# Kernel optimization log

Measured on AMD Instinct MI355X. Metric: run time of the kernel, lower is better.

The kernel has to match this reference:

```python
import jax, jax.numpy as jnp
import numpy as np

K = 20          # neighbors
M = 8           # weight-bank size per layer
EPS = 1e-5      # BatchNorm eps


def _bn(x, axes):
    # training-mode BatchNorm at init (gamma=1, beta=0), biased variance like torch
    mu = x.mean(axes, keepdims=True)
    var = x.var(axes, keepdims=True)
    return (x - mu) * jax.lax.rsqrt(var + EPS)


def _gather(feat, idx):
    # feat [B,N,C], idx [B,N,K] -> neighbor features [B,N,K,C]
    return jax.vmap(lambda f, i: f[i])(feat, idx)


def _knn_idx(x):
    # x [B,C,N]; pairwise_distance = -||xi||^2 + 2 xi.xj - ||xj||^2 (neg sq dist)
    sq = jnp.sum(x * x, axis=1)                      # [B,N]
    inner = jnp.einsum('bcn,bcm->bnm', x, x)          # [B,N,N]
    pd = 2.0 * inner - sq[:, :, None] - sq[:, None, :]
    return jax.lax.top_k(pd, K)[1]                    # [B,N,K]


def _scorenet(xyz, w1, w2, b):
    # xyz [B,N,K,6]; 1x1 Conv2d == channel-last matmul; BN2d over (B,N,K)
    h = jax.nn.relu(_bn(xyz @ w1, (0, 1, 2)))         # [B,N,K,16]
    s = h @ w2 + b                                    # [B,N,K,M]
    return jax.nn.softmax(s, axis=-1) + 0.5           # softmax over m, bias=0.5


def _paconv(feat, idx, ker, score):
    # feat [B,N,C]; ker [2C, M*O]; score [B,N,K,M]
    # torch: point = concat(x,x) @ ker -> [B,N,M,O]; center = x @ ker[:C]
    # assemble_dgcnn (assign_score_withk, aggregate='sum'):
    #   out[b,n,o] = sum_{k,m} score[b,n,k,m] * (point[b, idx[b,n,k], m, o] - center[b, n, m, o])
    C = feat.shape[-1]
    k3 = ker.reshape(2 * C, M, -1)
    Wa, Wb = k3[:C], k3[C:]                           # point uses Wa+Wb (x repeated); center uses Wa
    nf = _gather(feat, idx)                           # [B,N,K,C]
    T = jnp.einsum('bnkm,bnkc->bnmc', score, nf)      # score-weighted neighbor feats
    out = jnp.einsum('bnmc,cmo->bno', T, Wa + Wb)
    out = out - jnp.einsum('bnm,bnc,cmo->bno', score.sum(2), feat, Wa)
    return jax.nn.relu(_bn(out, (0, 1)))              # BN1d over (B,N), channel-last


def setup_inputs() -> dict:
    key = jax.random.key(0)
    ks = jax.random.split(key, 18)
    B, N = 32, 1024
    dims = [(3, 64), (64, 64), (64, 128), (128, 256)]
    d = {"x": jax.random.normal(ks[0], (B, 3, N), dtype=jnp.float32)}
    for i, (ci, co) in enumerate(dims):
        scale = (2.0 / (2 * ci)) ** 0.5  # kaiming_normal over fan_in=2*ci
        d[f"mat{i+1}"] = jax.random.normal(ks[1 + i], (2 * ci, M * co), dtype=jnp.float32) * scale
        d[f"sn{i+1}_w1"] = jax.random.normal(ks[5 + i], (6, 16), dtype=jnp.float32) * 0.4
        d[f"sn{i+1}_w2"] = jax.random.normal(ks[9 + i], (16, M), dtype=jnp.float32) * 0.25
        d[f"sn{i+1}_b"] = jnp.zeros((M,), dtype=jnp.float32)
    d["conv5_w"] = jax.random.normal(ks[13], (512, 1024), dtype=jnp.float32) * 0.04
    d["lin1_w"] = jax.random.normal(ks[14], (2048, 512), dtype=jnp.float32) * 0.02
    d["lin2_w"] = jax.random.normal(ks[15], (512, 256), dtype=jnp.float32) * 0.04
    d["lin3_w"] = jax.random.normal(ks[16], (256, 40), dtype=jnp.float32) * 0.06
    d["lin3_b"] = jnp.zeros((40,), dtype=jnp.float32)
    return d


def reference(x, mat1, mat2, mat3, mat4,
              sn1_w1, sn1_w2, sn1_b, sn2_w1, sn2_w2, sn2_b,
              sn3_w1, sn3_w2, sn3_b, sn4_w1, sn4_w2, sn4_b,
              conv5_w, lin1_w, lin2_w, lin3_w, lin3_b):
    idx = _knn_idx(x)                                  # [B,N,K]
    xT = jnp.swapaxes(x, 1, 2)                         # [B,N,3]
    nx = _gather(xT, idx)                              # [B,N,K,3]
    xyz = jnp.concatenate([nx - xT[:, :, None, :], nx], axis=-1)  # [B,N,K,6]

    p1 = _paconv(xT, idx, mat1, _scorenet(xyz, sn1_w1, sn1_w2, sn1_b))  # [B,N,64]
    p2 = _paconv(p1, idx, mat2, _scorenet(xyz, sn2_w1, sn2_w2, sn2_b))  # [B,N,64]
    p3 = _paconv(p2, idx, mat3, _scorenet(xyz, sn3_w1, sn3_w2, sn3_b))  # [B,N,128]
    p4 = _paconv(p3, idx, mat4, _scorenet(xyz, sn4_w1, sn4_w2, sn4_b))  # [B,N,256]

    p = jnp.concatenate([p1, p2, p3, p4], axis=-1)     # [B,N,512]
    p = jax.nn.relu(_bn(p @ conv5_w, (0, 1)))          # [B,N,1024]
    g = jnp.concatenate([p.max(axis=1), p.mean(axis=1)], axis=-1)  # [B,2048]
    h = jax.nn.relu(_bn(g @ lin1_w, (0,)))             # [B,512] (dropout = identity)
    h = jax.nn.relu(_bn(h @ lin2_w, (0,)))             # [B,256]
    return h @ lin3_w + lin3_b                         # [B,40]
```

## Files before the change

kernel.cpp:

```cpp
#include <hip/hip_runtime.h>
#include <cstdint>
#include <cstddef>

static constexpr int Bc  = 32;
static constexpr int Nc  = 1024;
static constexpr int Kc  = 20;
static constexpr int Mc  = 8;
static constexpr int BNc = Bc * Nc;
static constexpr int BNKc = BNc * Kc;

typedef __attribute__((ext_vector_type(4))) float f32x4;
typedef _Float16 f16x8 __attribute__((ext_vector_type(8)));

__device__ inline short f2h(float v) { _Float16 h = (_Float16)v; return __builtin_bit_cast(short, h); }
__device__ inline float h2f(short s) { return (float)__builtin_bit_cast(_Float16, s); }

__global__ void zero_kernel(float* p, int n) {
  int gid = blockIdx.x * blockDim.x + threadIdx.x;
  if (gid < n) p[gid] = 0.f;
}

__global__ __launch_bounds__(256) void knn_kernel(const float* __restrict__ x,
                                                  int* __restrict__ idxout) {
  int wv = threadIdx.x >> 6;
  int bn = blockIdx.x * 4 + wv;
  int b = bn >> 10, n = bn & (Nc - 1);
  int lane = threadIdx.x & 63;
  const float* xb = x + (size_t)b * 3 * Nc;
  float cx = xb[n], cy = xb[Nc + n], cz = xb[2 * Nc + n];
  float sqc = cx * cx + cy * cy + cz * cz;
  float d[16];
#pragma unroll
  for (int j = 0; j < 16; j++) {
    int m2 = j * 64 + lane;
    float xm = xb[m2], ym = xb[Nc + m2], zm = xb[2 * Nc + m2];
    d[j] = 2.f * (cx * xm + cy * ym + cz * zm) - sqc - (xm * xm + ym * ym + zm * zm);
  }
  int* out = idxout + (size_t)bn * Kc;
  for (int kk = 0; kk < Kc; kk++) {
    float bd = d[0]; int bj = 0;
#pragma unroll
    for (int j = 1; j < 16; j++)
      if (d[j] > bd) { bd = d[j]; bj = j; }
    int bm = bj * 64 + lane;
#pragma unroll
    for (int off = 32; off; off >>= 1) {
      float od = __shfl_down(bd, off);
      int   om = __shfl_down(bm, off);
      if (od > bd || (od == bd && om < bm)) { bd = od; bm = om; }
    }
    bm = __shfl(bm, 0);
    if (lane == 0) out[kk] = bm;
    int bmj = bm >> 6;
    bool mine = (bm & 63) == lane;
#pragma unroll
    for (int j = 0; j < 16; j++)
      if (mine && j == bmj) d[j] = -3e38f;
  }
}

__global__ __launch_bounds__(256) void xt_kernel(const float* __restrict__ x,
                                                 float* __restrict__ xT) {
  int gid = blockIdx.x * blockDim.x + threadIdx.x;
  int c = gid % 3;
  int bn = gid / 3;
  int b = bn >> 10, n = bn & (Nc - 1);
  xT[gid] = x[((size_t)b * 3 + c) * Nc + n];
}

__device__ inline void xyz_at(const float* __restrict__ xT, const int* __restrict__ idx,
                              int e, float v[6]) {
  int bn = e / Kc;
  int b = bn >> 10;
  int nb = idx[e];
  const float* pc = xT + (size_t)bn * 3;
  const float* pn = xT + ((size_t)(b << 10) + nb) * 3;
#pragma unroll
  for (int c = 0; c < 3; c++) { float nv = pn[c]; v[c] = nv - pc[c]; v[3 + c] = nv; }
}

__global__ __launch_bounds__(256) void xyz_stats_kernel(const float* __restrict__ xT,
                                                        const int* __restrict__ idx,
                                                        float* __restrict__ accum) {
  __shared__ float sPart[4 * 42];
  int tid = threadIdx.x;
  int gid = blockIdx.x * 256 + tid;
  float a[42];
#pragma unroll
  for (int t = 0; t < 42; t++) a[t] = 0.f;
  for (int i = 0; i < 8; i++) {
    float v[6];
    xyz_at(xT, idx, gid + i * 81920, v);
#pragma unroll
    for (int c = 0; c < 6; c++) a[c] += v[c];
    int t = 6;
#pragma unroll
    for (int c = 0; c < 6; c++)
#pragma unroll
      for (int d = 0; d < 6; d++) a[t++] += v[c] * v[d];
  }
  int lane = tid & 63, wid = tid >> 6;
#pragma unroll
  for (int t = 0; t < 42; t++) {
    float v = a[t];
#pragma unroll
    for (int off = 32; off; off >>= 1) v += __shfl_down(v, off);
    if (lane == 0) sPart[wid * 42 + t] = v;
  }
  __syncthreads();
  if (tid < 42) {
    float s = sPart[tid] + sPart[42 + tid] + sPart[84 + tid] + sPart[126 + tid];
    atomicAdd(&accum[tid], s);
  }
}

__global__ void snstats_kernel(const float* __restrict__ accum,
                               const float* __restrict__ w1a, const float* __restrict__ w1b,
                               const float* __restrict__ w1c, const float* __restrict__ w1d,
                               float* __restrict__ snstats) {
  int t = threadIdx.x;
  int l = t >> 4, j = t & 15;
  const float* w1 = (l == 0) ? w1a : (l == 1) ? w1b : (l == 2) ? w1c : w1d;
  const float invc = 1.f / (float)BNKc;
  float wj[6];
  float mu = 0.f;
#pragma unroll
  for (int c = 0; c < 6; c++) { wj[c] = w1[c * 16 + j]; mu += accum[c] * invc * wj[c]; }
  float e2 = 0.f;
#pragma unroll
  for (int c = 0; c < 6; c++)
#pragma unroll
    for (int d = 0; d < 6; d++) e2 += wj[c] * wj[d] * (accum[6 + c * 6 + d] * invc);
  float var = e2 - mu * mu;
  snstats[t * 2] = mu;
  snstats[t * 2 + 1] = rsqrtf(var + 1e-5f);
}

__global__ __launch_bounds__(256) void score_kernel(const float* __restrict__ xT,
                                                    const int* __restrict__ idx,
                                                    const float* __restrict__ w1,
                                                    const float* __restrict__ w2,
                                                    const float* __restrict__ bias,
                                                    const float* __restrict__ snst,
                                                    float* __restrict__ score) {
  __shared__ float sW1[96], sW2[128], sB[8], sMu[16], sRs[16];
  int tid = threadIdx.x;
  if (tid < 96) sW1[tid] = w1[tid];
  else if (tid < 224) sW2[tid - 96] = w2[tid - 96];
  else if (tid < 232) sB[tid - 224] = bias[tid - 224];
  else if (tid < 248) { sMu[tid - 232] = snst[(tid - 232) * 2]; sRs[tid - 232] = snst[(tid - 232) * 2 + 1]; }
  __syncthreads();
  int e = blockIdx.x * 256 + tid;
  float v[6];
  xyz_at(xT, idx, e, v);
  float h[16];
#pragma unroll
  for (int j = 0; j < 16; j++) {
    float a = 0.f;
#pragma unroll
    for (int c = 0; c < 6; c++) a += v[c] * sW1[c * 16 + j];
    a = (a - sMu[j]) * sRs[j];
    h[j] = a > 0.f ? a : 0.f;
  }
  float s[8];
  float mx = -3e38f;
#pragma unroll
  for (int m = 0; m < 8; m++) {
    float a = sB[m];
#pragma unroll
    for (int j = 0; j < 16; j++) a += h[j] * sW2[j * 8 + m];
    s[m] = a;
    mx = fmaxf(mx, a);
  }
  float sum = 0.f;
#pragma unroll
  for (int m = 0; m < 8; m++) { s[m] = expf(s[m] - mx); sum += s[m]; }
  float inv = 1.f / sum;
#pragma unroll
  for (int m = 0; m < 8; m++) score[(size_t)e * 8 + m] = s[m] * inv + 0.5f;
}

template <int C, int Co, int MH>
__global__ __launch_bounds__(256) void paconv_kernel(
    const float* __restrict__ feat, int fstride,
    const float* __restrict__ ker,
    const float* __restrict__ score,
    const int* __restrict__ idx,
    float* __restrict__ outp, int ostride) {
  constexpr int PT = 8;
  constexpr int MS = Mc / MH;
  __shared__ float sX[PT][2 * MH * C];
  __shared__ float sSc[PT * Kc * Mc];
  __shared__ int sIdx[PT * Kc];
  __shared__ float sFc[PT][C];
  __shared__ float sSum[PT][Mc];

  int tid = threadIdx.x;
  int pbase = blockIdx.x * PT;
  int bN = pbase & ~(Nc - 1);

  for (int e = tid; e < PT * Kc; e += 256) sIdx[e] = idx[(size_t)pbase * Kc + e];
  for (int e = tid; e < PT * Kc * Mc; e += 256) sSc[e] = score[(size_t)pbase * Kc * Mc + e];
  for (int e = tid; e < PT * C; e += 256) {
    int p = e / C, c = e - p * C;
    sFc[p][c] = feat[(size_t)(pbase + p) * fstride + c];
  }
  __syncthreads();
  for (int e = tid; e < PT * Mc; e += 256) {
    int p = e >> 3, m = e & 7;
    float s = 0.f;
#pragma unroll
    for (int k = 0; k < Kc; k++) s += sSc[p * Kc * Mc + k * Mc + m];
    sSum[p][m] = s;
  }
  __syncthreads();

  constexpr int OG = Co;
  constexpr int PG = 256 / OG;
  constexpr int PPT = PT / PG;
  int o = tid % OG;
  int pg = tid / OG;
  float acc[PPT];
#pragma unroll
  for (int i = 0; i < PPT; i++) acc[i] = 0.f;

  for (int ms = 0; ms < MS; ms++) {
    int mb = ms * MH;
    for (int e = tid; e < PT * C; e += 256) {
      int p = e / C, c = e - p * C;
      float t[MH];
#pragma unroll
      for (int mm = 0; mm < MH; mm++) t[mm] = 0.f;
      const float* sc = &sSc[p * Kc * Mc + mb];
      for (int k = 0; k < Kc; k++) {
        float v = feat[(size_t)(bN + sIdx[p * Kc + k]) * fstride + c];
#pragma unroll
        for (int mm = 0; mm < MH; mm++) t[mm] += sc[k * Mc + mm] * v;
      }
      float fc = sFc[p][c];
#pragma unroll
      for (int mm = 0; mm < MH; mm++) {
        sX[p][mm * C + c] = t[mm] - sSum[p][mb + mm] * fc;
        sX[p][MH * C + mm * C + c] = t[mm];
      }
    }
    __syncthreads();
#pragma unroll
    for (int mm = 0; mm < MH; mm++) {
      int m = mb + mm;
      const float* kerm = ker + (size_t)m * Co + o;
      for (int c = 0; c < C; c++) {
        float wA = kerm[(size_t)c * (Mc * Co)];
        float wB = kerm[(size_t)(C + c) * (Mc * Co)];
        int r = mm * C + c;
#pragma unroll
        for (int i = 0; i < PPT; i++) {
          int p = pg * PPT + i;
          acc[i] += sX[p][r] * wA;
          acc[i] += sX[p][MH * C + r] * wB;
        }
      }
    }
    __syncthreads();
  }

#pragma unroll
  for (int i = 0; i < PPT; i++) {
    int p = pg * PPT + i;
    outp[(size_t)(pbase + p) * ostride + o] = acc[i];
  }
}

template <int C>
__global__ __launch_bounds__(256) void gather_kernel(
    const short* __restrict__ pb, int coff,
    const float* __restrict__ score,
    const int* __restrict__ idx,
    short* __restrict__ TU, int p0) {
  constexpr int PT = 256 / C;
  __shared__ float sSc[PT][Kc][Mc];
  __shared__ int   sIdx[PT][Kc];
  __shared__ float sSum[PT][Mc];
  int tid = threadIdx.x;
  int pbase = p0 + blockIdx.x * PT;
  int bbase = pbase & ~(Nc - 1);
  for (int e = tid; e < PT * Kc * Mc; e += 256) (&sSc[0][0][0])[e] = score[(size_t)pbase * Kc * Mc + e];
  for (int e = tid; e < PT * Kc; e += 256) (&sIdx[0][0])[e] = idx[(size_t)pbase * Kc + e];
  __syncthreads();
  if (tid < PT * Mc) {
    int p = tid >> 3, m = tid & 7;
    float s = 0.f;
#pragma unroll
    for (int k = 0; k < Kc; k++) s += sSc[p][k][m];
    sSum[p][m] = s;
  }
  __syncthreads();
  int p = tid / C, c = tid - p * C;
  float t[Mc];
#pragma unroll
  for (int m = 0; m < Mc; m++) t[m] = 0.f;
  for (int k = 0; k < Kc; k++) {
    float v = h2f(pb[(size_t)(bbase + sIdx[p][k]) * 512 + coff + c]);
#pragma unroll
    for (int m = 0; m < Mc; m++) t[m] += sSc[p][k][m] * v;
  }
  float fc = h2f(pb[(size_t)(pbase + p) * 512 + coff + c]);
  short* rowp = TU + (size_t)(pbase + p - p0) * (2 * Mc * C);
#pragma unroll
  for (int m = 0; m < Mc; m++) {
    rowp[m * C + c]          = f2h(t[m] - sSum[p][m] * fc);
    rowp[Mc * C + m * C + c] = f2h(t[m]);
  }
}

__global__ __launch_bounds__(256) void kerconv_kernel(const float* __restrict__ ker,
                                                      short* __restrict__ Bt,
                                                      int C, int Co, int total) {
  int gid = blockIdx.x * 256 + threadIdx.x;
  if (gid >= total) return;
  int RT = 2 * Mc * C;
  int o = gid / RT, r = gid - o * RT;
  int half = r / (Mc * C);
  int mc = r - half * Mc * C;
  int m = mc / C, c = mc - m * C;
  Bt[gid] = f2h(ker[(size_t)(half * C + c) * (Mc * Co) + m * Co + o]);
}

__global__ __launch_bounds__(256) void w5conv_kernel(const float* __restrict__ W,
                                                     short* __restrict__ Wt) {
  int gid = blockIdx.x * 256 + threadIdx.x;
  int o = gid >> 9, k = gid & 511;
  Wt[gid] = f2h(W[(size_t)k * 1024 + o]);
}

template <int BM, int BN, bool OUT_HALF>
__global__ __launch_bounds__(256) void gemm_kernel(
    const short* __restrict__ A,
    const short* __restrict__ Bt,
    int K,
    void* __restrict__ Cout, int ldc) {
  constexpr int BK = 64;
  constexpr int FM = (BM + 31) / 32;
  constexpr int FN = BN / 32;
  __shared__ short sA[BM * BK];
  __shared__ short sB[BN * BK];
  int tid = threadIdx.x;
  int lane = tid & 63, wv = tid >> 6;
  int wrow = (wv & 1) * (BM / 2);
  int wcol = (wv >> 1) * (BN / 2);
  int bm0 = blockIdx.x * BM;
  int bn0 = blockIdx.y * BN;
  int r15 = lane & 15, quad = lane >> 4;
  int swz = r15 & 7;

  constexpr int FMW = BM / 32 >= 1 ? BM / 32 : 1;
  f32x4 acc[FMW][FN];
#pragma unroll
  for (int fm = 0; fm < FMW; fm++)
#pragma unroll
    for (int fn = 0; fn < FN; fn++) acc[fm][fn] = (f32x4){0.f, 0.f, 0.f, 0.f};

  for (int k0 = 0; k0 < K; k0 += BK) {
#pragma unroll
    for (int i = 0; i < (BM * BK / 8) / 256; i++) {
      int cb = i * 256 + wv * 64;
      int chunk = cb + lane;
      int row = chunk >> 3, kc = (chunk & 7) ^ (row & 7);
      const short* g = A + (size_t)(bm0 + row) * K + k0 + kc * 8;
      __builtin_amdgcn_global_load_lds((const __attribute__((address_space(1))) void*)g,
                                       (__attribute__((address_space(3))) void*)&sA[cb * 8],
                                       16, 0, 0);
    }
#pragma unroll
    for (int i = 0; i < (BN * BK / 8) / 256; i++) {
      int cb = i * 256 + wv * 64;
      int chunk = cb + lane;
      int row = chunk >> 3, kc = (chunk & 7) ^ (row & 7);
      const short* g = Bt + (size_t)(bn0 + row) * K + k0 + kc * 8;
      __builtin_amdgcn_global_load_lds((const __attribute__((address_space(1))) void*)g,
                                       (__attribute__((address_space(3))) void*)&sB[cb * 8],
                                       16, 0, 0);
    }
    __syncthreads();
#pragma unroll
    for (int kk = 0; kk < BK; kk += 32) {
      f16x8 af[FMW], bf[FN];
      int ccol = (kk >> 3) + quad;
#pragma unroll
      for (int fm = 0; fm < FMW; fm++)
        af[fm] = *(const f16x8*)&sA[(wrow + fm * 16 + r15) * BK + ((ccol ^ swz) * 8)];
#pragma unroll
      for (int fn = 0; fn < FN; fn++)
        bf[fn] = *(const f16x8*)&sB[(wcol + fn * 16 + r15) * BK + ((ccol ^ swz) * 8)];
#pragma unroll
      for (int fm = 0; fm < FMW; fm++)
#pragma unroll
        for (int fn = 0; fn < FN; fn++)
          acc[fm][fn] = __builtin_amdgcn_mfma_f32_16x16x32_f16(af[fm], bf[fn], acc[fm][fn], 0, 0, 0);
    }
    __syncthreads();
  }

#pragma unroll
  for (int fn = 0; fn < FN; fn++) {
    int col = bn0 + wcol + fn * 16 + r15;
#pragma unroll
    for (int fm = 0; fm < FMW; fm++) {
      int rowb = bm0 + wrow + fm * 16 + quad * 4;
#pragma unroll
      for (int r = 0; r < 4; r++) {
        float v = acc[fm][fn][r];
        if constexpr (OUT_HALF) ((short*)Cout)[(size_t)(rowb + r) * ldc + col] = f2h(v);
        else                    ((float*)Cout)[(size_t)(rowb + r) * ldc + col] = v;
      }
    }
  }
}

template <bool IS_HALF>
__global__ __launch_bounds__(256) void bnstats_kernel(const void* __restrict__ pre,
                                                      int Co,
                                                      float* __restrict__ bnslots) {
  __shared__ float sS[4][64], sQ[4][64];
  int tid = threadIdx.x;
  int c = tid & 63, tg = tid >> 6;
  int ch = blockIdx.x * 64 + c;
  int row0 = blockIdx.y * 1024 + tg * 256;
  float s = 0.f, q = 0.f;
  if constexpr (IS_HALF) {
    const short* p = (const short*)pre + (size_t)row0 * Co + ch;
#pragma unroll 4
    for (int r = 0; r < 256; r++) {
      float v = h2f(p[(size_t)r * Co]);
      s += v; q += v * v;
    }
  } else {
    const float* p = (const float*)pre + (size_t)row0 * Co + ch;
#pragma unroll 4
    for (int r = 0; r < 256; r++) {
      float v = p[(size_t)r * Co];
      s += v; q += v * v;
    }
  }
  sS[tg][c] = s; sQ[tg][c] = q;
  __syncthreads();
  if (tid < 64) {
    float ts = sS[0][tid] + sS[1][tid] + sS[2][tid] + sS[3][tid];
    float tq = sQ[0][tid] + sQ[1][tid] + sQ[2][tid] + sQ[3][tid];
    int chh = blockIdx.x * 64 + tid;
    bnslots[(chh * 32 + blockIdx.y) * 2 + 0] = ts;
    bnslots[(chh * 32 + blockIdx.y) * 2 + 1] = tq;
  }
}

__global__ void bnfinalize_kernel(const float* __restrict__ slots,
                                  float* __restrict__ bnmr, int Co) {
  int ch = blockIdx.x * blockDim.x + threadIdx.x;
  if (ch >= Co) return;
  float s = 0.f, q = 0.f;
#pragma unroll 4
  for (int i = 0; i < 32; i++) { s += slots[(ch * 32 + i) * 2]; q += slots[(ch * 32 + i) * 2 + 1]; }
  float mu = s / (float)BNc;
  float var = q / (float)BNc - mu * mu;
  bnmr[ch * 2] = mu;
  bnmr[ch * 2 + 1] = rsqrtf(var + 1e-5f);
}

__global__ __launch_bounds__(256) void bnapply_kernel(const float* __restrict__ pre,
                                                      int Co, const float* __restrict__ bnmr,
                                                      short* __restrict__ pb, int coff) {
  int gid = blockIdx.x * 256 + threadIdx.x;
  int row = gid / Co, ch = gid - row * Co;
  float mu = bnmr[ch * 2], rs = bnmr[ch * 2 + 1];
  float v = (pre[gid] - mu) * rs;
  pb[(size_t)row * 512 + coff + ch] = f2h(v > 0.f ? v : 0.f);
}

__global__ __launch_bounds__(512) void g2_kernel(const short* __restrict__ pre,
                                                 const float* __restrict__ bnmr,
                                                 float* __restrict__ g) {
  int b = blockIdx.x, nch = blockIdx.y;
  int tid = threadIdx.x;
  int ch0 = 2 * tid;
  float mu0 = bnmr[ch0 * 2],     rs0 = bnmr[ch0 * 2 + 1];
  float mu1 = bnmr[ch0 * 2 + 2], rs1 = bnmr[ch0 * 2 + 3];
  const uint32_t* p32 = (const uint32_t*)(pre + (size_t)b * 1024 * 1024 + (size_t)nch * 128 * 1024);
  float mx0 = 0.f, mx1 = 0.f, sm0 = 0.f, sm1 = 0.f;
#pragma unroll 4
  for (int n = 0; n < 128; n++) {
    uint32_t u = p32[n * 512 + tid];
    float v0 = (h2f((short)(u & 0xffff)) - mu0) * rs0;
    float v1 = (h2f((short)(u >> 16))    - mu1) * rs1;
    v0 = v0 > 0.f ? v0 : 0.f;
    v1 = v1 > 0.f ? v1 : 0.f;
    mx0 = fmaxf(mx0, v0); mx1 = fmaxf(mx1, v1);
    sm0 += v0; sm1 += v1;
  }
  int* gi = (int*)g;
  atomicMax(&gi[b * 2048 + ch0], __float_as_int(mx0));
  atomicMax(&gi[b * 2048 + ch0 + 1], __float_as_int(mx1));
  atomicAdd(&g[b * 2048 + 1024 + ch0], sm0 * (1.f / 1024.f));
  atomicAdd(&g[b * 2048 + 1024 + ch0 + 1], sm1 * (1.f / 1024.f));
}

__global__ __launch_bounds__(256) void linsplit_kernel(const float* __restrict__ A,
                                                       const float* __restrict__ W,
                                                       float* __restrict__ out,
                                                       int Kdim, int Cols, int kchunk) {
  int j = blockIdx.x * 256 + threadIdx.x;
  if (j >= Cols) return;
  int b = blockIdx.y;
  int k0 = blockIdx.z * kchunk;
  const float* a = A + (size_t)b * Kdim + k0;
  const float* w = W + (size_t)k0 * Cols + j;
  float acc = 0.f;
#pragma unroll 4
  for (int i = 0; i < kchunk; i++) acc += a[i] * w[(size_t)i * Cols];
  atomicAdd(&out[b * Cols + j], acc);
}

__global__ __launch_bounds__(256) void biasinit_kernel(const float* __restrict__ bias,
                                                       float* __restrict__ out, int Cols, int n) {
  int gid = blockIdx.x * 256 + threadIdx.x;
  if (gid < n) out[gid] = bias[gid % Cols];
}

__global__ __launch_bounds__(256) void lin_bn_kernel(float* __restrict__ X, int Cols) {
  int j = blockIdx.x * 256 + threadIdx.x;
  if (j >= Cols) return;
  float s = 0.f, q = 0.f;
#pragma unroll
  for (int b = 0; b < 32; b++) { float v = X[b * Cols + j]; s += v; q += v * v; }
  float mu = s * (1.f / 32.f);
  float var = q * (1.f / 32.f) - mu * mu;
  float rs = rsqrtf(var + 1e-5f);
#pragma unroll
  for (int b = 0; b < 32; b++) {
    float v = (X[b * Cols + j] - mu) * rs;
    X[b * Cols + j] = v > 0.f ? v : 0.f;
  }
}

extern "C" void kernel_launch(void* const* d_in, const int* in_sizes, int n_in,
                              void* d_out, int out_size, void* d_ws, size_t ws_size,
                              hipStream_t stream) {
  (void)in_sizes; (void)n_in; (void)out_size; (void)ws_size;
  const float* x      = (const float*)d_in[0];
  const float* mat1   = (const float*)d_in[1];
  const float* sn1_w1 = (const float*)d_in[2];
  const float* sn1_w2 = (const float*)d_in[3];
  const float* sn1_b  = (const float*)d_in[4];
  const float* mat2   = (const float*)d_in[5];
  const float* sn2_w1 = (const float*)d_in[6];
  const float* sn2_w2 = (const float*)d_in[7];
  const float* sn2_b  = (const float*)d_in[8];
  const float* mat3   = (const float*)d_in[9];
  const float* sn3_w1 = (const float*)d_in[10];
  const float* sn3_w2 = (const float*)d_in[11];
  const float* sn3_b  = (const float*)d_in[12];
  const float* mat4   = (const float*)d_in[13];
  const float* sn4_w1 = (const float*)d_in[14];
  const float* sn4_w2 = (const float*)d_in[15];
  const float* sn4_b  = (const float*)d_in[16];
  const float* conv5w = (const float*)d_in[17];
  const float* lin1w  = (const float*)d_in[18];
  const float* lin2w  = (const float*)d_in[19];
  const float* lin3w  = (const float*)d_in[20];
  const float* lin3b  = (const float*)d_in[21];
  float* out = (float*)d_out;

  char* ws = (char*)d_ws;
  size_t cur = 0;
  auto alloc = [&](size_t bytes) {
    size_t r = cur;
    cur += (bytes + 1023) & ~(size_t)1023;
    return r;
  };
  size_t off_idx   = alloc((size_t)BNKc * 4);
  size_t off_xT    = alloc((size_t)BNc * 3 * 4);
  size_t off_st    = alloc((size_t)157888 * 4);
  size_t off_score = alloc((size_t)BNKc * 8 * 4);
  size_t off_pre   = alloc((size_t)BNc * 256 * 4);
  size_t off_pb    = alloc((size_t)BNc * 512 * 2);
  size_t off_kb    = alloc((size_t)1048576);
  size_t off_TU    = alloc((size_t)BNc * 1024 * 2);

  int*   idx   = (int*)(ws + off_idx);
  float* xT    = (float*)(ws + off_xT);
  float* stats = (float*)(ws + off_st);
  float* score = (float*)(ws + off_score);
  float* pre   = (float*)(ws + off_pre);
  short* pb    = (short*)(ws + off_pb);
  short* kb    = (short*)(ws + off_kb);
  short* TU    = (short*)(ws + off_TU);
  short* pre5  = (short*)(ws + off_TU);

  float* xyzacc  = stats;
  float* snstats = stats + 64;
  float* bnslots = stats + 192;
  float* bnmr    = stats + 65728;
  float* g       = stats + 67776;
  float* h1      = stats + 133312;
  float* h2      = stats + 149696;

  zero_kernel<<<1, 64, 0, stream>>>(xyzacc, 64);
  knn_kernel<<<BNc / 4, 256, 0, stream>>>(x, idx);
  xt_kernel<<<BNc * 3 / 256, 256, 0, stream>>>(x, xT);
  xyz_stats_kernel<<<320, 256, 0, stream>>>(xT, idx, xyzacc);
  snstats_kernel<<<1, 64, 0, stream>>>(xyzacc, sn1_w1, sn2_w1, sn3_w1, sn4_w1, snstats);

  score_kernel<<<BNKc / 256, 256, 0, stream>>>(xT, idx, sn1_w1, sn1_w2, sn1_b, snstats + 0, score);
  paconv_kernel<3, 64, 8><<<BNc / 8, 256, 0, stream>>>(xT, 3, mat1, score, idx, pre, 64);
  bnstats_kernel<false><<<dim3(1, 32), 256, 0, stream>>>(pre, 64, bnslots);
  bnfinalize_kernel<<<1, 64, 0, stream>>>(bnslots, bnmr, 64);
  bnapply_kernel<<<BNc * 64 / 256, 256, 0, stream>>>(pre, 64, bnmr, pb, 0);

  score_kernel<<<BNKc / 256, 256, 0, stream>>>(xT, idx, sn2_w1, sn2_w2, sn2_b, snstats + 32, score);
  gather_kernel<64><<<BNc / 4, 256, 0, stream>>>(pb, 0, score, idx, TU, 0);
  kerconv_kernel<<<64 * 1024 / 256, 256, 0, stream>>>(mat2, kb, 64, 64, 64 * 1024);
  gemm_kernel<32, 64, false><<<dim3(1024, 1), 256, 0, stream>>>(TU, kb, 1024, pre, 64);
  bnstats_kernel<false><<<dim3(1, 32), 256, 0, stream>>>(pre, 64, bnslots);
  bnfinalize_kernel<<<1, 64, 0, stream>>>(bnslots, bnmr, 64);
  bnapply_kernel<<<BNc * 64 / 256, 256, 0, stream>>>(pre, 64, bnmr, pb, 64);

  score_kernel<<<BNKc / 256, 256, 0, stream>>>(xT, idx, sn3_w1, sn3_w2, sn3_b, snstats + 64, score);
  gather_kernel<64><<<BNc / 4, 256, 0, stream>>>(pb, 64, score, idx, TU, 0);
  kerconv_kernel<<<128 * 1024 / 256, 256, 0, stream>>>(mat3, kb, 64, 128, 128 * 1024);
  gemm_kernel<32, 128, false><<<dim3(1024, 1), 256, 0, stream>>>(TU, kb, 1024, pre, 128);
  bnstats_kernel<false><<<dim3(2, 32), 256, 0, stream>>>(pre, 128, bnslots);
  bnfinalize_kernel<<<1, 128, 0, stream>>>(bnslots, bnmr, 128);
  bnapply_kernel<<<BNc * 128 / 256, 256, 0, stream>>>(pre, 128, bnmr, pb, 128);

  score_kernel<<<BNKc / 256, 256, 0, stream>>>(xT, idx, sn4_w1, sn4_w2, sn4_b, snstats + 96, score);
  kerconv_kernel<<<256 * 2048 / 256, 256, 0, stream>>>(mat4, kb, 128, 256, 256 * 2048);
  for (int ch = 0; ch < 2; ch++) {
    int p0 = ch * 16384;
    gather_kernel<128><<<16384 / 2, 256, 0, stream>>>(pb, 128, score, idx, TU, p0);
    gemm_kernel<32, 128, false><<<dim3(512, 2), 256, 0, stream>>>(TU, kb, 2048,
                                                                  pre + (size_t)p0 * 256, 256);
  }
  bnstats_kernel<false><<<dim3(4, 32), 256, 0, stream>>>(pre, 256, bnslots);
  bnfinalize_kernel<<<1, 256, 0, stream>>>(bnslots, bnmr, 256);
  bnapply_kernel<<<BNc * 256 / 256, 256, 0, stream>>>(pre, 256, bnmr, pb, 256);

  w5conv_kernel<<<524288 / 256, 256, 0, stream>>>(conv5w, kb);
  gemm_kernel<128, 128, true><<<dim3(256, 8), 256, 0, stream>>>(pb, kb, 512, pre5, 1024);
  bnstats_kernel<true><<<dim3(16, 32), 256, 0, stream>>>(pre5, 1024, bnslots);
  bnfinalize_kernel<<<4, 256, 0, stream>>>(bnslots, bnmr, 1024);

  zero_kernel<<<256, 256, 0, stream>>>(g, 65536);
  g2_kernel<<<dim3(32, 8), 512, 0, stream>>>(pre5, bnmr, g);

  zero_kernel<<<64, 256, 0, stream>>>(h1, 16384);
  linsplit_kernel<<<dim3(2, 32, 8), 256, 0, stream>>>(g, lin1w, h1, 2048, 512, 256);
  lin_bn_kernel<<<2, 256, 0, stream>>>(h1, 512);
  zero_kernel<<<32, 256, 0, stream>>>(h2, 8192);
  linsplit_kernel<<<dim3(1, 32, 4), 256, 0, stream>>>(h1, lin2w, h2, 512, 256, 128);
  lin_bn_kernel<<<1, 256, 0, stream>>>(h2, 256);
  biasinit_kernel<<<5, 256, 0, stream>>>(lin3b, out, 40, 1280);
  linsplit_kernel<<<dim3(1, 32, 2), 256, 0, stream>>>(h2, lin3w, out, 256, 40, 128);
}
```

Before: 830.9 us.

## Rebuild center term inside GEMM from features and score sums instead of materializing

```diff
diff --git a/kernel.cpp b/kernel.cpp
--- a/kernel.cpp
+++ b/kernel.cpp
@@ -276,13 +276,13 @@
     const short* __restrict__ pb, int coff,
     const float* __restrict__ score,
     const int* __restrict__ idx,
-    short* __restrict__ TU, int p0) {
+    short* __restrict__ T, short* __restrict__ sumb) {
   constexpr int PT = 256 / C;
+  constexpr int KH = Mc * C;
   __shared__ float sSc[PT][Kc][Mc];
   __shared__ int   sIdx[PT][Kc];
-  __shared__ float sSum[PT][Mc];
   int tid = threadIdx.x;
-  int pbase = p0 + blockIdx.x * PT;
+  int pbase = blockIdx.x * PT;
   int bbase = pbase & ~(Nc - 1);
   for (int e = tid; e < PT * Kc * Mc; e += 256) (&sSc[0][0][0])[e] = score[(size_t)pbase * Kc * Mc + e];
   for (int e = tid; e < PT * Kc; e += 256) (&sIdx[0][0])[e] = idx[(size_t)pbase * Kc + e];
@@ -292,9 +292,8 @@
     float s = 0.f;
 #pragma unroll
     for (int k = 0; k < Kc; k++) s += sSc[p][k][m];
-    sSum[p][m] = s;
-  }
-  __syncthreads();
+    sumb[(size_t)(pbase + p) * 8 + m] = f2h(s);
+  }
   int p = tid / C, c = tid - p * C;
   float t[Mc];
 #pragma unroll
@@ -304,26 +303,29 @@
 #pragma unroll
     for (int m = 0; m < Mc; m++) t[m] += sSc[p][k][m] * v;
   }
-  float fc = h2f(pb[(size_t)(pbase + p) * 512 + coff + c]);
-  short* rowp = TU + (size_t)(pbase + p - p0) * (2 * Mc * C);
-#pragma unroll
-  for (int m = 0; m < Mc; m++) {
-    rowp[m * C + c]          = f2h(t[m] - sSum[p][m] * fc);
-    rowp[Mc * C + m * C + c] = f2h(t[m]);
-  }
-}
-
-__global__ __launch_bounds__(256) void kerconv_kernel(const float* __restrict__ ker,
-                                                      short* __restrict__ Bt,
-                                                      int C, int Co, int total) {
+  short* rowp = T + (size_t)(pbase + p) * KH;
+#pragma unroll
+  for (int m = 0; m < Mc; m++) rowp[m * C + c] = f2h(t[m]);
+}
+
+__global__ __launch_bounds__(256) void kerconv_r1_kernel(const float* __restrict__ ker,
+                                                         short* __restrict__ Bt,
+                                                         int C, int Co, int total) {
   int gid = blockIdx.x * 256 + threadIdx.x;
   if (gid >= total) return;
-  int RT = 2 * Mc * C;
-  int o = gid / RT, r = gid - o * RT;
-  int half = r / (Mc * C);
-  int mc = r - half * Mc * C;
-  int m = mc / C, c = mc - m * C;
-  Bt[gid] = f2h(ker[(size_t)(half * C + c) * (Mc * Co) + m * Co + o]);
+  int KH = Mc * C;
+  int K2 = 2 * KH;
+  int o = gid / K2, r = gid - o * K2;
+  float v;
+  if (r < KH) {
+    int m = r / C, c = r - m * C;
+    v = ker[(size_t)c * (Mc * Co) + m * Co + o] + ker[(size_t)(C + c) * (Mc * Co) + m * Co + o];
+  } else {
+    int r2 = r - KH;
+    int m = r2 / C, c = r2 - m * C;
+    v = -ker[(size_t)c * (Mc * Co) + m * Co + o];
+  }
+  Bt[gid] = f2h(v);
 }
 
 __global__ __launch_bounds__(256) void w5conv_kernel(const float* __restrict__ W,
@@ -340,8 +342,8 @@
     int K,
     void* __restrict__ Cout, int ldc) {
   constexpr int BK = 64;
-  constexpr int FM = (BM + 31) / 32;
   constexpr int FN = BN / 32;
+  constexpr int FMW = BM / 32;
   __shared__ short sA[BM * BK];
   __shared__ short sB[BN * BK];
   int tid = threadIdx.x;
@@ -353,7 +355,6 @@
   int r15 = lane & 15, quad = lane >> 4;
   int swz = r15 & 7;
 
-  constexpr int FMW = BM / 32 >= 1 ? BM / 32 : 1;
   f32x4 acc[FMW][FN];
 #pragma unroll
   for (int fm = 0; fm < FMW; fm++)
@@ -413,6 +414,115 @@
         if constexpr (OUT_HALF) ((short*)Cout)[(size_t)(rowb + r) * ldc + col] = f2h(v);
         else                    ((float*)Cout)[(size_t)(rowb + r) * ldc + col] = v;
       }
+    }
+  }
+}
+
+template <int BM, int BN, int C>
+__global__ __launch_bounds__(256) void gemm_r1_kernel(
+    const short* __restrict__ T,
+    const short* __restrict__ Bt,
+    const short* __restrict__ pb, int coff,
+    const short* __restrict__ sumb,
+    float* __restrict__ Cout, int ldc) {
+  constexpr int BK = 64;
+  constexpr int KH = Mc * C;
+  constexpr int K2 = 2 * KH;
+  constexpr int FN = BN / 32;
+  constexpr int FMW = BM / 32;
+  __shared__ short sA[BM * BK];
+  __shared__ short sB[BN * BK];
+  __shared__ short sFc[BM * C];
+  __shared__ short sSm[BM * 8];
+  int tid = threadIdx.x;
+  int lane = tid & 63, wv = tid >> 6;
+  int wrow = (wv & 1) * (BM / 2);
+  int wcol = (wv >> 1) * (BN / 2);
+  int bm0 = blockIdx.x * BM;
+  int bn0 = blockIdx.y * BN;
+  int r15 = lane & 15, quad = lane >> 4;
+  int swz = r15 & 7;
+
+  for (int e = tid; e < BM * C; e += 256) {
+    int p = e / C, c = e - p * C;
+    sFc[e] = pb[(size_t)(bm0 + p) * 512 + coff + c];
+  }
+  for (int e = tid; e < BM * 8; e += 256) sSm[e] = sumb[(size_t)bm0 * 8 + e];
+
+  f32x4 acc[FMW][FN];
+#pragma unroll
+  for (int fm = 0; fm < FMW; fm++)
+#pragma unroll
+    for (int fn = 0; fn < FN; fn++) acc[fm][fn] = (f32x4){0.f, 0.f, 0.f, 0.f};
+  __syncthreads();
+
+  for (int k0 = 0; k0 < K2; k0 += BK) {
+    if (k0 < KH) {
+#pragma unroll
+      for (int i = 0; i < (BM * BK / 8) / 256; i++) {
+        int cb = i * 256 + wv * 64;
+        int chunk = cb + lane;
+        int row = chunk >> 3, kc = (chunk & 7) ^ (row & 7);
+        const short* g = T + (size_t)(bm0 + row) * KH + k0 + kc * 8;
+        __builtin_amdgcn_global_load_lds((const __attribute__((address_space(1))) void*)g,
+                                         (__attribute__((address_space(3))) void*)&sA[cb * 8],
+                                         16, 0, 0);
+      }
+    } else {
+#pragma unroll
+      for (int i = 0; i < (BM * BK / 8) / 256; i++) {
+        int cb = i * 256 + wv * 64;
+        int chunk = cb + lane;
+        int row = chunk >> 3, kc = (chunk & 7) ^ (row & 7);
+        int kb = (k0 - KH) + kc * 8;
+        int m = kb / C, c = kb - m * C;
+        _Float16 sm = __builtin_bit_cast(_Float16, sSm[row * 8 + m]);
+        f16x8 fcv = *(const f16x8*)&sFc[row * C + c];
+        f16x8 val;
+#pragma unroll
+        for (int j = 0; j < 8; j++) val[j] = sm * fcv[j];
+        *(f16x8*)&sA[chunk * 8] = val;
+      }
+    }
+#pragma unroll
+    for (int i = 0; i < (BN * BK / 8) / 256; i++) {
+      int cb = i * 256 + wv * 64;
+      int chunk = cb + lane;
+      int row = chunk >> 3, kc = (chunk & 7) ^ (row & 7);
+      const short* g = Bt + (size_t)(bn0 + row) * K2 + k0 + kc * 8;
+      __builtin_amdgcn_global_load_lds((const __attribute__((address_space(1))) void*)g,
+                                       (__attribute__((address_space(3))) void*)&sB[cb * 8],
+                                       16, 0, 0);
+    }
+    __syncthreads();
+#pragma unroll
+    for (int kk = 0; kk < BK; kk += 32) {
+      f16x8 af[FMW], bf[FN];
+      int ccol = (kk >> 3) + quad;
+#pragma unroll
+      for (int fm = 0; fm < FMW; fm++)
+        af[fm] = *(const f16x8*)&sA[(wrow + fm * 16 + r15) * BK + ((ccol ^ swz) * 8)];
+#pragma unroll
+      for (int fn = 0; fn < FN; fn++)
+        bf[fn] = *(const f16x8*)&sB[(wcol + fn * 16 + r15) * BK + ((ccol ^ swz) * 8)];
+#pragma unroll
+      for (int fm = 0; fm < FMW; fm++)
+#pragma unroll
+        for (int fn = 0; fn < FN; fn++)
+          acc[fm][fn] = __builtin_amdgcn_mfma_f32_16x16x32_f16(af[fm], bf[fn], acc[fm][fn], 0, 0, 0);
+    }
+    __syncthreads();
+  }
+
+#pragma unroll
+  for (int fn = 0; fn < FN; fn++) {
+    int col = bn0 + wcol + fn * 16 + r15;
+#pragma unroll
+    for (int fm = 0; fm < FMW; fm++) {
+      int rowb = bm0 + wrow + fm * 16 + quad * 4;
+#pragma unroll
+      for (int r = 0; r < 4; r++)
+        Cout[(size_t)(rowb + r) * ldc + col] = acc[fm][fn][r];
     }
   }
 }
@@ -579,6 +689,7 @@
   size_t off_idx   = alloc((size_t)BNKc * 4);
   size_t off_xT    = alloc((size_t)BNc * 3 * 4);
   size_t off_st    = alloc((size_t)157888 * 4);
+  size_t off_sum   = alloc((size_t)BNc * 8 * 2);
   size_t off_score = alloc((size_t)BNKc * 8 * 4);
   size_t off_pre   = alloc((size_t)BNc * 256 * 4);
   size_t off_pb    = alloc((size_t)BNc * 512 * 2);
@@ -588,11 +699,12 @@
   int*   idx   = (int*)(ws + off_idx);
   float* xT    = (float*)(ws + off_xT);
   float* stats = (float*)(ws + off_st);
+  short* sumb  = (short*)(ws + off_sum);
   float* score = (float*)(ws + off_score);
   float* pre   = (float*)(ws + off_pre);
   short* pb    = (short*)(ws + off_pb);
   short* kb    = (short*)(ws + off_kb);
-  short* TU    = (short*)(ws + off_TU);
+  short* T     = (short*)(ws + off_TU);
   short* pre5  = (short*)(ws + off_TU);
 
   float* xyzacc  = stats;
@@ -616,29 +728,25 @@
   bnapply_kernel<<<BNc * 64 / 256, 256, 0, stream>>>(pre, 64, bnmr, pb, 0);
 
   score_kernel<<<BNKc / 256, 256, 0, stream>>>(xT, idx, sn2_w1, sn2_w2, sn2_b, snstats + 32, score);
-  gather_kernel<64><<<BNc / 4, 256, 0, stream>>>(pb, 0, score, idx, TU, 0);
-  kerconv_kernel<<<64 * 1024 / 256, 256, 0, stream>>>(mat2, kb, 64, 64, 64 * 1024);
-  gemm_kernel<32, 64, false><<<dim3(1024, 1), 256, 0, stream>>>(TU, kb, 1024, pre, 64);
+  gather_kernel<64><<<BNc / 4, 256, 0, stream>>>(pb, 0, score, idx, T, sumb);
+  kerconv_r1_kernel<<<64 * 1024 / 256, 256, 0, stream>>>(mat2, kb, 64, 64, 64 * 1024);
+  gemm_r1_kernel<64, 64, 64><<<dim3(512, 1), 256, 0, stream>>>(T, kb, pb, 0, sumb, pre, 64);
   bnstats_kernel<false><<<dim3(1, 32), 256, 0, stream>>>(pre, 64, bnslots);
   bnfinalize_kernel<<<1, 64, 0, stream>>>(bnslots, bnmr, 64);
   bnapply_kernel<<<BNc * 64 / 256, 256, 0, stream>>>(pre, 64, bnmr, pb, 64);
 
   score_kernel<<<BNKc / 256, 256, 0, stream>>>(xT, idx, sn3_w1, sn3_w2, sn3_b, snstats + 64, score);
-  gather_kernel<64><<<BNc / 4, 256, 0, stream>>>(pb, 64, score, idx, TU, 0);
-  kerconv_kernel<<<128 * 1024 / 256, 256, 0, stream>>>(mat3, kb, 64, 128, 128 * 1024);
-  gemm_kernel<32, 128, false><<<dim3(1024, 1), 256, 0, stream>>>(TU, kb, 1024, pre, 128);
+  gather_kernel<64><<<BNc / 4, 256, 0, stream>>>(pb, 64, score, idx, T, sumb);
+  kerconv_r1_kernel<<<128 * 1024 / 256, 256, 0, stream>>>(mat3, kb, 64, 128, 128 * 1024);
+  gemm_r1_kernel<64, 128, 64><<<dim3(512, 1), 256, 0, stream>>>(T, kb, pb, 64, sumb, pre, 128);
   bnstats_kernel<false><<<dim3(2, 32), 256, 0, stream>>>(pre, 128, bnslots);
   bnfinalize_kernel<<<1, 128, 0, stream>>>(bnslots, bnmr, 128);
   bnapply_kernel<<<BNc * 128 / 256, 256, 0, stream>>>(pre, 128, bnmr, pb, 128);
 
   score_kernel<<<BNKc / 256, 256, 0, stream>>>(xT, idx, sn4_w1, sn4_w2, sn4_b, snstats + 96, score);
-  kerconv_kernel<<<256 * 2048 / 256, 256, 0, stream>>>(mat4, kb, 128, 256, 256 * 2048);
-  for (int ch = 0; ch < 2; ch++) {
-    int p0 = ch * 16384;
-    gather_kernel<128><<<16384 / 2, 256, 0, stream>>>(pb, 128, score, idx, TU, p0);
-    gemm_kernel<32, 128, false><<<dim3(512, 2), 256, 0, stream>>>(TU, kb, 2048,
-                                                                  pre + (size_t)p0 * 256, 256);
-  }
+  gather_kernel<128><<<BNc / 2, 256, 0, stream>>>(pb, 128, score, idx, T, sumb);
+  kerconv_r1_kernel<<<256 * 2048 / 256, 256, 0, stream>>>(mat4, kb, 128, 256, 256 * 2048);
+  gemm_r1_kernel<64, 128, 128><<<dim3(512, 2), 256, 0, stream>>>(T, kb, pb, 128, sumb, pre, 256);
   bnstats_kernel<false><<<dim3(4, 32), 256, 0, stream>>>(pre, 256, bnslots);
   bnfinalize_kernel<<<1, 256, 0, stream>>>(bnslots, bnmr, 256);
   bnapply_kernel<<<BNc * 256 / 256, 256, 0, stream>>>(pre, 256, bnmr, pb, 256);
```

New measurement: 826.7 us. No clear change (-0.5%).
